# Kernel tuning notes

Measured on AMD Instinct MI355X. Metric: run time of the kernel, lower is better.

## Reference

```python
import jax, jax.numpy as jnp
import numpy as np

B, S, D, H, E, K = 4, 2048, 1024, 2048, 8, 2
MU, GAMMA, LN_EPS = 0.7, 1.0, 1e-5


def setup_inputs() -> dict:
    key = jax.random.key(0)
    ks = jax.random.split(key, 8)
    inv_d = 1.0 / np.sqrt(D)
    inv_h = 1.0 / np.sqrt(H)
    return {
        "x": jax.random.normal(ks[0], (B, S, D), dtype=jnp.float32),
        "momentum": jax.random.normal(ks[1], (B, S, D), dtype=jnp.float32),
        "Wg": jax.random.normal(ks[2], (D, E), dtype=jnp.float32) * inv_d,
        "bg": jnp.zeros((E,), dtype=jnp.float32),
        "W1": jax.random.normal(ks[3], (E, D, H), dtype=jnp.float32) * inv_d,
        "b1": jnp.zeros((E, H), dtype=jnp.float32),
        "W2": jax.random.normal(ks[4], (E, H, D), dtype=jnp.float32) * inv_h,
        "b2": jnp.zeros((E, D), dtype=jnp.float32),
        "ln_g": jnp.ones((D,), dtype=jnp.float32),
        "ln_b": jnp.zeros((D,), dtype=jnp.float32),
    }


def reference(x, momentum, Wg, bg, W1, b1, W2, b2, ln_g, ln_b):
    # --- TopKGate: linear router, softmax over top-k logits, zeros elsewhere ---
    logits = jnp.einsum("bsd,de->bse", x, Wg) + bg            # [B,S,E]
    top_v, top_i = jax.lax.top_k(logits, K)                    # [B,S,K]
    top_w = jax.nn.softmax(top_v, axis=-1)                     # [B,S,K]
    gates = jnp.sum(jax.nn.one_hot(top_i, E, dtype=x.dtype) * top_w[..., None], axis=-2)  # [B,S,E]

    # --- Dense all-expert FFN (faithful to the original per-expert loop) ---
    h = jax.nn.relu(jnp.einsum("bsd,edh->bseh", x, W1) + b1)   # [B,S,E,H]
    eo = jnp.einsum("bseh,ehd->bsed", h, W2) + b2              # [B,S,E,D]
    expert_outputs = jnp.einsum("bse,bsed->bsd", gates, eo)    # [B,S,D]

    # --- Momentum update + residual + LayerNorm ---
    new_momentum = -expert_outputs + MU * momentum
    out = x + GAMMA * new_momentum
    mean = jnp.mean(out, axis=-1, keepdims=True)
    var = jnp.mean(jnp.square(out - mean), axis=-1, keepdims=True)
    out = (out - mean) * jax.lax.rsqrt(var + LN_EPS) * ln_g + ln_b
    return out, new_momentum
```

## Files before the change

kernel.cpp:

```cpp
#include <hip/hip_runtime.h>

#define TT 8192
#define DD 1024
#define HHH 2048
#define EE 8
#define MUf 0.7f
#define GAMMAf 1.0f
#define LNEPS 1e-5f

typedef __bf16 bf16x8 __attribute__((ext_vector_type(8)));
typedef float floatx4 __attribute__((ext_vector_type(4)));

__device__ __forceinline__ unsigned short f2bf(float f) {
  unsigned u = __float_as_uint(f);
  u += 0x7FFFu + ((u >> 16) & 1u);
  return (unsigned short)(u >> 16);
}
__device__ __forceinline__ float bf2f(unsigned short u) {
  return __uint_as_float(((unsigned)u) << 16);
}
__device__ __forceinline__ void load_lds16(const void* g, void* l) {
  __builtin_amdgcn_global_load_lds(
      (__attribute__((address_space(1))) void*)g,
      (__attribute__((address_space(3))) void*)l,
      16, 0, 0);
}

__global__ __launch_bounds__(256) void cvt_router_kernel(
    const float* __restrict__ x, const float* __restrict__ Wg, const float* __restrict__ bg,
    unsigned short* __restrict__ xb,
    int* __restrict__ pair_e, float* __restrict__ pair_w) {
  int tid = threadIdx.x;
  size_t gi = (size_t)blockIdx.x * 2048 + (size_t)tid * 8;
  const float4* s = (const float4*)(x + gi);
  float4 a = s[0], b = s[1];
  unsigned r0 = f2bf(a.x) | ((unsigned)f2bf(a.y) << 16);
  unsigned r1 = f2bf(a.z) | ((unsigned)f2bf(a.w) << 16);
  unsigned r2 = f2bf(b.x) | ((unsigned)f2bf(b.y) << 16);
  unsigned r3 = f2bf(b.z) | ((unsigned)f2bf(b.w) << 16);
  ((uint4*)xb)[blockIdx.x * 256 + tid] = make_uint4(r0, r1, r2, r3);

  float xa[8] = {a.x, a.y, a.z, a.w, b.x, b.y, b.z, b.w};
  int d0 = (tid & 127) * 8;
  const float* wbase = Wg + (size_t)d0 * EE;
  float acc[EE];
#pragma unroll
  for (int e = 0; e < EE; ++e) acc[e] = 0.f;
#pragma unroll
  for (int i = 0; i < 8; ++i) {
    float4 w0 = *(const float4*)(wbase + i * EE);
    float4 w1 = *(const float4*)(wbase + i * EE + 4);
    acc[0] += xa[i] * w0.x; acc[1] += xa[i] * w0.y;
    acc[2] += xa[i] * w0.z; acc[3] += xa[i] * w0.w;
    acc[4] += xa[i] * w1.x; acc[5] += xa[i] * w1.y;
    acc[6] += xa[i] * w1.z; acc[7] += xa[i] * w1.w;
  }
#pragma unroll
  for (int e = 0; e < EE; ++e) {
#pragma unroll
    for (int off = 32; off > 0; off >>= 1) acc[e] += __shfl_xor(acc[e], off);
  }
  __shared__ float rs[4][EE];
  int wv = tid >> 6;
  if ((tid & 63) == 0) {
#pragma unroll
    for (int e = 0; e < EE; ++e) rs[wv][e] = acc[e];
  }
  __syncthreads();
  if ((tid & 127) == 0) {
    int half = tid >> 7;
    int t = blockIdx.x * 2 + half;
    float v[EE];
#pragma unroll
    for (int e = 0; e < EE; ++e) v[e] = rs[2 * half][e] + rs[2 * half + 1][e] + bg[e];
    int i0 = 0;
#pragma unroll
    for (int e = 1; e < EE; ++e) if (v[e] > v[i0]) i0 = e;
    int i1 = (i0 == 0) ? 1 : 0;
#pragma unroll
    for (int e = 0; e < EE; ++e) if (e != i0 && v[e] > v[i1]) i1 = e;
    float w1e = __expf(v[i1] - v[i0]);
    float inv = 1.f / (1.f + w1e);
    pair_e[2 * t] = i0;     pair_w[2 * t] = inv;
    pair_e[2 * t + 1] = i1; pair_w[2 * t + 1] = w1e * inv;
  }
}

__global__ __launch_bounds__(256) void count_kernel(const int* __restrict__ pair_e,
                                                    int* __restrict__ counts) {
  __shared__ int lh[EE];
  int tid = threadIdx.x;
  if (tid < EE) lh[tid] = 0;
  __syncthreads();
  int p = blockIdx.x * 256 + tid;
  atomicAdd(&lh[pair_e[p]], 1);
  __syncthreads();
  if (tid < EE) atomicAdd(&counts[tid], lh[tid]);
}

__global__ void prefix_kernel(const int* __restrict__ counts, int* __restrict__ offs,
                              int* __restrict__ cursor) {
  if (threadIdx.x == 0) {
    int s = 0;
    for (int e = 0; e < EE; ++e) { offs[e] = s; cursor[e] = s; s += counts[e]; }
    offs[EE] = s;
  }
}

__global__ __launch_bounds__(256) void scatter_kernel(const int* __restrict__ pair_e,
                                                      int* __restrict__ cursor,
                                                      int* __restrict__ pair_rows) {
  __shared__ int lh[EE];
  __shared__ int lb[EE];
  int tid = threadIdx.x;
  if (tid < EE) lh[tid] = 0;
  __syncthreads();
  int p = blockIdx.x * 256 + tid;
  int e = pair_e[p];
  int r = atomicAdd(&lh[e], 1);
  __syncthreads();
  if (tid < EE) lb[tid] = atomicAdd(&cursor[tid], lh[tid]);
  __syncthreads();
  pair_rows[lb[e] + r] = p;
}

__global__ __launch_bounds__(256) void transpose_cvt_kernel(const float* __restrict__ in,
                                                            unsigned short* __restrict__ out,
                                                            int R, int C) {
  __shared__ float tile[32][33];
  int e = blockIdx.z;
  const float* src = in + (size_t)e * R * C;
  unsigned short* dst = out + (size_t)e * R * C;
  int c0 = blockIdx.x * 32, r0 = blockIdx.y * 32;
  int tx = threadIdx.x, ty = threadIdx.y;
#pragma unroll
  for (int i = 0; i < 32; i += 8)
    tile[ty + i][tx] = src[(size_t)(r0 + ty + i) * C + (c0 + tx)];
  __syncthreads();
#pragma unroll
  for (int i = 0; i < 32; i += 8)
    dst[(size_t)(c0 + ty + i) * R + (r0 + tx)] = f2bf(tile[tx][ty + i]);
}

template <int MODE>
__global__ __launch_bounds__(256, 2) void moe_gemm_kernel(
    const unsigned short* __restrict__ Amat, const unsigned short* __restrict__ Bmat,
    const float* __restrict__ bias, const int* __restrict__ offsets,
    const int* __restrict__ pair_rows, const float* __restrict__ pair_w,
    unsigned short* __restrict__ Out, int Kd, int Nd) {
  int e = blockIdx.z;
  int off = offsets[e];
  int cnt = offsets[e + 1] - off;
  int mt = blockIdx.y;
  if (mt * 128 >= cnt) return;
  int n0 = blockIdx.x * 128;
  int tid = threadIdx.x;

  __shared__ unsigned short As[128 * 32];
  __shared__ unsigned short Bs[128 * 32];

  const unsigned short* Bex = Bmat + (size_t)e * Nd * Kd;

  const unsigned short* aptr[2];
  const unsigned short* bptr[2];
#pragma unroll
  for (int P = 0; P < 2; ++P) {
    int row = P * 64 + (tid >> 2);
    int kpart = (tid & 3) * 8;
    int s = mt * 128 + row;
    if (s >= cnt) s = cnt - 1;
    int gr = (MODE == 0) ? (pair_rows[off + s] >> 1) : (off + s);
    aptr[P] = Amat + (size_t)gr * Kd + kpart;
    bptr[P] = Bex + (size_t)(n0 + row) * Kd + kpart;
  }

  int lane = tid & 63, wid = tid >> 6;
  int wm = (wid >> 1) * 64, wn = (wid & 1) * 64;
  int lr = lane & 15, lkb = (lane >> 4) * 8;

  floatx4 acc[4][4];
#pragma unroll
  for (int m = 0; m < 4; ++m) {
#pragma unroll
    for (int n = 0; n < 4; ++n) acc[m][n] = (floatx4){0.f, 0.f, 0.f, 0.f};
  }

  for (int k0 = 0; k0 < Kd; k0 += 32) {
    __syncthreads();
#pragma unroll
    for (int P = 0; P < 2; ++P) {
      load_lds16(aptr[P] + k0, As + P * 2048 + tid * 8);
      load_lds16(bptr[P] + k0, Bs + P * 2048 + tid * 8);
    }
    __syncthreads();
    bf16x8 af[4], bfr[4];
#pragma unroll
    for (int m = 0; m < 4; ++m) af[m] = *(const bf16x8*)(As + (wm + m * 16 + lr) * 32 + lkb);
#pragma unroll
    for (int n = 0; n < 4; ++n) bfr[n] = *(const bf16x8*)(Bs + (wn + n * 16 + lr) * 32 + lkb);
#pragma unroll
    for (int m = 0; m < 4; ++m) {
#pragma unroll
      for (int n = 0; n < 4; ++n)
        acc[m][n] = __builtin_amdgcn_mfma_f32_16x16x32_bf16(af[m], bfr[n], acc[m][n], 0, 0, 0);
    }
  }

  int rem = cnt - mt * 128;
  if (rem > 128) rem = 128;
#pragma unroll
  for (int m = 0; m < 4; ++m) {
#pragma unroll
    for (int j = 0; j < 4; ++j) {
      int lrr = wm + m * 16 + ((lane >> 4) << 2) + j;
      if (lrr < rem) {
        int s = mt * 128 + lrr;
        size_t orow;
        float scale = 1.f;
        if (MODE == 0) {
          orow = (size_t)(off + s) * Nd;
        } else {
          int p = pair_rows[off + s];
          orow = (size_t)p * Nd;
          scale = pair_w[p];
        }
#pragma unroll
        for (int n = 0; n < 4; ++n) {
          int col = n0 + wn + n * 16 + lr;
          float v = acc[m][n][j] + bias[e * Nd + col];
          if (MODE == 0) v = fmaxf(v, 0.f);
          else v *= scale;
          Out[orow + col] = f2bf(v);
        }
      }
    }
  }
}

__global__ __launch_bounds__(256) void final_kernel(
    const float* __restrict__ x, const float* __restrict__ mom,
    const unsigned short* __restrict__ pairout, const float* __restrict__ ln_g,
    const float* __restrict__ ln_b, float* __restrict__ outp, float* __restrict__ nmp) {
  int t = blockIdx.x, tid = threadIdx.x;
  int d0 = tid * 4;
  size_t rowoff = (size_t)t * DD;
  const unsigned short* p0 = pairout + (size_t)(2 * t) * DD;
  const unsigned short* p1 = p0 + DD;
  float4 xv = *(const float4*)(x + rowoff + d0);
  float4 mv = *(const float4*)(mom + rowoff + d0);
  ushort4 u0 = *(const ushort4*)(p0 + d0);
  ushort4 u1 = *(const ushort4*)(p1 + d0);
  float eo[4] = {bf2f(u0.x) + bf2f(u1.x), bf2f(u0.y) + bf2f(u1.y),
                 bf2f(u0.z) + bf2f(u1.z), bf2f(u0.w) + bf2f(u1.w)};
  float xa[4] = {xv.x, xv.y, xv.z, xv.w};
  float ma[4] = {mv.x, mv.y, mv.z, mv.w};
  float o[4], nm[4];
  float s1 = 0.f, s2 = 0.f;
#pragma unroll
  for (int j = 0; j < 4; ++j) {
    nm[j] = MUf * ma[j] - eo[j];
    o[j] = xa[j] + GAMMAf * nm[j];
    s1 += o[j];
    s2 += o[j] * o[j];
  }
  *(float4*)(nmp + rowoff + d0) = make_float4(nm[0], nm[1], nm[2], nm[3]);
#pragma unroll
  for (int off = 32; off > 0; off >>= 1) {
    s1 += __shfl_xor(s1, off);
    s2 += __shfl_xor(s2, off);
  }
  __shared__ float rs[8];
  int wid = tid >> 6, lane = tid & 63;
  if (lane == 0) { rs[wid] = s1; rs[4 + wid] = s2; }
  __syncthreads();
  s1 = rs[0] + rs[1] + rs[2] + rs[3];
  s2 = rs[4] + rs[5] + rs[6] + rs[7];
  float mean = s1 * (1.f / DD);
  float var = s2 * (1.f / DD) - mean * mean;
  float rstd = rsqrtf(var + LNEPS);
  float4 g = *(const float4*)(ln_g + d0);
  float4 bb = *(const float4*)(ln_b + d0);
  float ga[4] = {g.x, g.y, g.z, g.w}, ba[4] = {bb.x, bb.y, bb.z, bb.w};
  float res[4];
#pragma unroll
  for (int j = 0; j < 4; ++j) res[j] = (o[j] - mean) * rstd * ga[j] + ba[j];
  *(float4*)(outp + rowoff + d0) = make_float4(res[0], res[1], res[2], res[3]);
}

extern "C" void kernel_launch(void* const* d_in, const int* in_sizes, int n_in,
                              void* d_out, int out_size, void* d_ws, size_t ws_size,
                              hipStream_t stream) {
  const float* x   = (const float*)d_in[0];
  const float* mom = (const float*)d_in[1];
  const float* Wg  = (const float*)d_in[2];
  const float* bg  = (const float*)d_in[3];
  const float* W1  = (const float*)d_in[4];
  const float* b1  = (const float*)d_in[5];
  const float* W2  = (const float*)d_in[6];
  const float* b2  = (const float*)d_in[7];
  const float* lng = (const float*)d_in[8];
  const float* lnb = (const float*)d_in[9];
  (void)in_sizes; (void)n_in; (void)out_size; (void)ws_size;
  float* outp = (float*)d_out;
  float* nmp  = outp + (size_t)TT * DD;

  char* base = (char*)d_ws;
  size_t off = 0;
  auto carve = [&](size_t bytes) {
    void* p = base + off;
    off += (bytes + 255) & ~(size_t)255;
    return p;
  };
  unsigned short* xb   = (unsigned short*)carve((size_t)TT * DD * 2);
  unsigned short* w1t  = (unsigned short*)carve((size_t)EE * HHH * DD * 2);
  unsigned short* w2t  = (unsigned short*)carve((size_t)EE * DD * HHH * 2);
  unsigned short* hbuf = (unsigned short*)carve((size_t)2 * TT * HHH * 2);
  unsigned short* pout = (unsigned short*)carve((size_t)2 * TT * DD * 2);
  int*   pair_e    = (int*)carve((size_t)2 * TT * 4);
  float* pair_w    = (float*)carve((size_t)2 * TT * 4);
  int*   pair_rows = (int*)carve((size_t)2 * TT * 4);
  int*   counts    = (int*)carve(256);
  int*   offs      = (int*)carve(256);
  int*   cursor    = (int*)carve(256);

  hipMemsetAsync(counts, 0, EE * sizeof(int), stream);
  cvt_router_kernel<<<TT / 2, 256, 0, stream>>>(x, Wg, bg, xb, pair_e, pair_w);
  count_kernel<<<(2 * TT) / 256, 256, 0, stream>>>(pair_e, counts);
  prefix_kernel<<<1, 64, 0, stream>>>(counts, offs, cursor);
  scatter_kernel<<<(2 * TT) / 256, 256, 0, stream>>>(pair_e, cursor, pair_rows);
  transpose_cvt_kernel<<<dim3(HHH / 32, DD / 32, EE), dim3(32, 8, 1), 0, stream>>>(W1, w1t, DD, HHH);
  transpose_cvt_kernel<<<dim3(DD / 32, HHH / 32, EE), dim3(32, 8, 1), 0, stream>>>(W2, w2t, HHH, DD);
  moe_gemm_kernel<0><<<dim3(HHH / 128, 128, EE), 256, 0, stream>>>(
      xb, w1t, b1, offs, pair_rows, pair_w, hbuf, DD, HHH);
  moe_gemm_kernel<1><<<dim3(DD / 128, 128, EE), 256, 0, stream>>>(
      hbuf, w2t, b2, offs, pair_rows, pair_w, pout, HHH, DD);
  final_kernel<<<TT, 256, 0, stream>>>(x, mom, pout, lng, lnb, outp, nmp);
}
```

Measured before the change: 354.5 us.

## Enlarge MoE GEMM tiles to 256x256x64 with double-buffered LDS prefetch

The grouped expert GEMM moves from 128x128 tiles with K-step 32 and 256 threads to 256x256 tiles with K-step 64 and 512 threads. Each wave now holds an 8x4 grid of MFMA accumulators. Global-to-LDS loads for the next K tile are issued before computing the current one, using two LDS buffers and one barrier per iteration. The aim is more operand reuse per byte loaded and load latency hidden behind MFMA work. The cost is 128KB of LDS per block, so only one block fits per CU and occupancy drops; the 128-byte LDS row stride may also cause more bank conflicts.

```diff
diff --git a/kernel.cpp b/kernel.cpp
--- a/kernel.cpp
+++ b/kernel.cpp
@@ -143,7 +143,7 @@
 }
 
 template <int MODE>
-__global__ __launch_bounds__(256, 2) void moe_gemm_kernel(
+__global__ __launch_bounds__(512, 2) void moe_gemm_kernel(
     const unsigned short* __restrict__ Amat, const unsigned short* __restrict__ Bmat,
     const float* __restrict__ bias, const int* __restrict__ offsets,
     const int* __restrict__ pair_rows, const float* __restrict__ pair_w,
@@ -152,69 +152,85 @@
   int off = offsets[e];
   int cnt = offsets[e + 1] - off;
   int mt = blockIdx.y;
-  if (mt * 128 >= cnt) return;
-  int n0 = blockIdx.x * 128;
+  if (mt * 256 >= cnt) return;
+  int n0 = blockIdx.x * 256;
   int tid = threadIdx.x;
-
-  __shared__ unsigned short As[128 * 32];
-  __shared__ unsigned short Bs[128 * 32];
+  int lane = tid & 63, wid = tid >> 6;
+
+  __shared__ unsigned short As[2][256 * 64];
+  __shared__ unsigned short Bs[2][256 * 64];
 
   const unsigned short* Bex = Bmat + (size_t)e * Nd * Kd;
 
-  const unsigned short* aptr[2];
-  const unsigned short* bptr[2];
-#pragma unroll
-  for (int P = 0; P < 2; ++P) {
-    int row = P * 64 + (tid >> 2);
-    int kpart = (tid & 3) * 8;
-    int s = mt * 128 + row;
-    if (s >= cnt) s = cnt - 1;
-    int gr = (MODE == 0) ? (pair_rows[off + s] >> 1) : (off + s);
-    aptr[P] = Amat + (size_t)gr * Kd + kpart;
-    bptr[P] = Bex + (size_t)(n0 + row) * Kd + kpart;
-  }
-
-  int lane = tid & 63, wid = tid >> 6;
-  int wm = (wid >> 1) * 64, wn = (wid & 1) * 64;
-  int lr = lane & 15, lkb = (lane >> 4) * 8;
-
-  floatx4 acc[4][4];
-#pragma unroll
-  for (int m = 0; m < 4; ++m) {
+  int c = lane & 7;
+  int rsub = wid * 8 + (lane >> 3);
+  const unsigned short* aptr[4];
+  const unsigned short* bptr[4];
+#pragma unroll
+  for (int s = 0; s < 4; ++s) {
+    int row = s * 64 + rsub;
+    int sa = mt * 256 + row;
+    if (sa >= cnt) sa = cnt - 1;
+    int gr = (MODE == 0) ? (pair_rows[off + sa] >> 1) : (off + sa);
+    aptr[s] = Amat + (size_t)gr * Kd + c * 8;
+    bptr[s] = Bex + (size_t)(n0 + row) * Kd + c * 8;
+  }
+
+  int wm = (wid >> 2) * 128, wn = (wid & 3) * 64;
+  int lr = lane & 15, lk = (lane >> 4) * 8;
+
+  floatx4 acc[8][4];
+#pragma unroll
+  for (int m = 0; m < 8; ++m)
 #pragma unroll
     for (int n = 0; n < 4; ++n) acc[m][n] = (floatx4){0.f, 0.f, 0.f, 0.f};
-  }
-
-  for (int k0 = 0; k0 < Kd; k0 += 32) {
-    __syncthreads();
-#pragma unroll
-    for (int P = 0; P < 2; ++P) {
-      load_lds16(aptr[P] + k0, As + P * 2048 + tid * 8);
-      load_lds16(bptr[P] + k0, Bs + P * 2048 + tid * 8);
+
+  int NT = Kd >> 6;
+#pragma unroll
+  for (int s = 0; s < 4; ++s) {
+    load_lds16(aptr[s], &As[0][(s * 64 + wid * 8) * 64] + lane * 8);
+    load_lds16(bptr[s], &Bs[0][(s * 64 + wid * 8) * 64] + lane * 8);
+  }
+  __syncthreads();
+
+  int buf = 0;
+  for (int kt = 0; kt < NT; ++kt) {
+    if (kt + 1 < NT) {
+      int ko = (kt + 1) * 64;
+#pragma unroll
+      for (int s = 0; s < 4; ++s) {
+        load_lds16(aptr[s] + ko, &As[buf ^ 1][(s * 64 + wid * 8) * 64] + lane * 8);
+        load_lds16(bptr[s] + ko, &Bs[buf ^ 1][(s * 64 + wid * 8) * 64] + lane * 8);
+      }
+    }
+#pragma unroll
+    for (int kk = 0; kk < 2; ++kk) {
+      bf16x8 af[8], bf[4];
+#pragma unroll
+      for (int m = 0; m < 8; ++m)
+        af[m] = *(const bf16x8*)(&As[buf][(wm + m * 16 + lr) * 64 + kk * 32 + lk]);
+#pragma unroll
+      for (int n = 0; n < 4; ++n)
+        bf[n] = *(const bf16x8*)(&Bs[buf][(wn + n * 16 + lr) * 64 + kk * 32 + lk]);
+#pragma unroll
+      for (int m = 0; m < 8; ++m)
+#pragma unroll
+        for (int n = 0; n < 4; ++n)
+          acc[m][n] = __builtin_amdgcn_mfma_f32_16x16x32_bf16(af[m], bf[n], acc[m][n], 0, 0, 0);
     }
     __syncthreads();
-    bf16x8 af[4], bfr[4];
-#pragma unroll
-    for (int m = 0; m < 4; ++m) af[m] = *(const bf16x8*)(As + (wm + m * 16 + lr) * 32 + lkb);
-#pragma unroll
-    for (int n = 0; n < 4; ++n) bfr[n] = *(const bf16x8*)(Bs + (wn + n * 16 + lr) * 32 + lkb);
-#pragma unroll
-    for (int m = 0; m < 4; ++m) {
-#pragma unroll
-      for (int n = 0; n < 4; ++n)
-        acc[m][n] = __builtin_amdgcn_mfma_f32_16x16x32_bf16(af[m], bfr[n], acc[m][n], 0, 0, 0);
-    }
-  }
-
-  int rem = cnt - mt * 128;
-  if (rem > 128) rem = 128;
-#pragma unroll
-  for (int m = 0; m < 4; ++m) {
+    buf ^= 1;
+  }
+
+  int rem = cnt - mt * 256;
+  if (rem > 256) rem = 256;
+#pragma unroll
+  for (int m = 0; m < 8; ++m) {
 #pragma unroll
     for (int j = 0; j < 4; ++j) {
       int lrr = wm + m * 16 + ((lane >> 4) << 2) + j;
       if (lrr < rem) {
-        int s = mt * 128 + lrr;
+        int s = mt * 256 + lrr;
         size_t orow;
         float scale = 1.f;
         if (MODE == 0) {
@@ -330,9 +346,9 @@
   scatter_kernel<<<(2 * TT) / 256, 256, 0, stream>>>(pair_e, cursor, pair_rows);
   transpose_cvt_kernel<<<dim3(HHH / 32, DD / 32, EE), dim3(32, 8, 1), 0, stream>>>(W1, w1t, DD, HHH);
   transpose_cvt_kernel<<<dim3(DD / 32, HHH / 32, EE), dim3(32, 8, 1), 0, stream>>>(W2, w2t, HHH, DD);
-  moe_gemm_kernel<0><<<dim3(HHH / 128, 128, EE), 256, 0, stream>>>(
+  moe_gemm_kernel<0><<<dim3(HHH / 256, 64, EE), 512, 0, stream>>>(
       xb, w1t, b1, offs, pair_rows, pair_w, hbuf, DD, HHH);
-  moe_gemm_kernel<1><<<dim3(DD / 128, 128, EE), 256, 0, stream>>>(
+  moe_gemm_kernel<1><<<dim3(DD / 256, 64, EE), 512, 0, stream>>>(
       hbuf, w2t, b2, offs, pair_rows, pair_w, pout, HHH, DD);
   final_kernel<<<TT, 256, 0, stream>>>(x, mom, pout, lng, lnb, outp, nmp);
 }
```

Result: slower. 419.7 us (+18.4%).

## Double-buffer LDS tiles, XOR-swizzle K chunks, raise occupancy in MoE GEMM

Applied to the files above, without the earlier changes.

The MoE GEMM kernel now keeps two LDS stages for the A and B tiles and prefetches the next K tile while MFMAs run on the current one, leaving one barrier per iteration instead of two. Global-to-LDS loads and fragment reads use an XOR swizzle of the 8-element K chunk with the row index to reduce LDS bank conflicts. Launch bounds rise from 2 to 4 blocks per SM to raise occupancy. LDS per block doubles to 32 KB, and the tighter register budget from the higher occupancy target could cause spills.

```diff
diff --git a/kernel.cpp b/kernel.cpp
--- a/kernel.cpp
+++ b/kernel.cpp
@@ -143,7 +143,7 @@
 }
 
 template <int MODE>
-__global__ __launch_bounds__(256, 2) void moe_gemm_kernel(
+__global__ __launch_bounds__(256, 4) void moe_gemm_kernel(
     const unsigned short* __restrict__ Amat, const unsigned short* __restrict__ Bmat,
     const float* __restrict__ bias, const int* __restrict__ offsets,
     const int* __restrict__ pair_rows, const float* __restrict__ pair_w,
@@ -155,55 +155,69 @@
   if (mt * 128 >= cnt) return;
   int n0 = blockIdx.x * 128;
   int tid = threadIdx.x;
-
-  __shared__ unsigned short As[128 * 32];
-  __shared__ unsigned short Bs[128 * 32];
+  int lane = tid & 63, wid = tid >> 6;
+
+  __shared__ unsigned short As[2][128 * 32];
+  __shared__ unsigned short Bs[2][128 * 32];
 
   const unsigned short* Bex = Bmat + (size_t)e * Nd * Kd;
 
+  int csw = (((tid & 3) ^ ((tid >> 2) & 3)) * 8);
   const unsigned short* aptr[2];
   const unsigned short* bptr[2];
 #pragma unroll
   for (int P = 0; P < 2; ++P) {
     int row = P * 64 + (tid >> 2);
-    int kpart = (tid & 3) * 8;
-    int s = mt * 128 + row;
-    if (s >= cnt) s = cnt - 1;
-    int gr = (MODE == 0) ? (pair_rows[off + s] >> 1) : (off + s);
-    aptr[P] = Amat + (size_t)gr * Kd + kpart;
-    bptr[P] = Bex + (size_t)(n0 + row) * Kd + kpart;
-  }
-
-  int lane = tid & 63, wid = tid >> 6;
+    int sa = mt * 128 + row;
+    if (sa >= cnt) sa = cnt - 1;
+    int gr = (MODE == 0) ? (pair_rows[off + sa] >> 1) : (off + sa);
+    aptr[P] = Amat + (size_t)gr * Kd + csw;
+    bptr[P] = Bex + (size_t)(n0 + row) * Kd + csw;
+  }
+
   int wm = (wid >> 1) * 64, wn = (wid & 1) * 64;
-  int lr = lane & 15, lkb = (lane >> 4) * 8;
+  int lr = lane & 15;
+  int t4 = lane >> 4;
+  int lka = ((t4 ^ (lr & 3)) * 8);
 
   floatx4 acc[4][4];
 #pragma unroll
-  for (int m = 0; m < 4; ++m) {
+  for (int m = 0; m < 4; ++m)
 #pragma unroll
     for (int n = 0; n < 4; ++n) acc[m][n] = (floatx4){0.f, 0.f, 0.f, 0.f};
-  }
-
-  for (int k0 = 0; k0 < Kd; k0 += 32) {
-    __syncthreads();
-#pragma unroll
-    for (int P = 0; P < 2; ++P) {
-      load_lds16(aptr[P] + k0, As + P * 2048 + tid * 8);
-      load_lds16(bptr[P] + k0, Bs + P * 2048 + tid * 8);
+
+  int NT = Kd >> 5;
+#pragma unroll
+  for (int P = 0; P < 2; ++P) {
+    load_lds16(aptr[P], &As[0][P * 2048] + tid * 8);
+    load_lds16(bptr[P], &Bs[0][P * 2048] + tid * 8);
+  }
+  __syncthreads();
+
+  int buf = 0;
+  for (int kt = 0; kt < NT; ++kt) {
+    if (kt + 1 < NT) {
+      int ko = (kt + 1) * 32;
+#pragma unroll
+      for (int P = 0; P < 2; ++P) {
+        load_lds16(aptr[P] + ko, &As[buf ^ 1][P * 2048] + tid * 8);
+        load_lds16(bptr[P] + ko, &Bs[buf ^ 1][P * 2048] + tid * 8);
+      }
     }
-    __syncthreads();
     bf16x8 af[4], bfr[4];
 #pragma unroll
-    for (int m = 0; m < 4; ++m) af[m] = *(const bf16x8*)(As + (wm + m * 16 + lr) * 32 + lkb);
-#pragma unroll
-    for (int n = 0; n < 4; ++n) bfr[n] = *(const bf16x8*)(Bs + (wn + n * 16 + lr) * 32 + lkb);
-#pragma unroll
-    for (int m = 0; m < 4; ++m) {
+    for (int m = 0; m < 4; ++m)
+      af[m] = *(const bf16x8*)(&As[buf][(wm + m * 16 + lr) * 32 + lka]);
+#pragma unroll
+    for (int n = 0; n < 4; ++n)
+      bfr[n] = *(const bf16x8*)(&Bs[buf][(wn + n * 16 + lr) * 32 + lka]);
+#pragma unroll
+    for (int m = 0; m < 4; ++m)
 #pragma unroll
       for (int n = 0; n < 4; ++n)
         acc[m][n] = __builtin_amdgcn_mfma_f32_16x16x32_bf16(af[m], bfr[n], acc[m][n], 0, 0, 0);
-    }
+    __syncthreads();
+    buf ^= 1;
   }
 
   int rem = cnt - mt * 128;
```

Result: no change. 359.9 us (+1.5%).
